# Kernel optimization log

Hardware: AMD Instinct MI355X
Metric: run time of the kernel (lower is better)

The kernel has to match this reference:

```python
import jax, jax.numpy as jnp
import numpy as np
import math

DIM = 1024
HEADS = 16
SEQ_LEN = 2048
NUM_PV = 32
HEAD_DIM = DIM // HEADS
EPS = 1e-5


def setup_inputs() -> dict:
    key = jax.random.key(0)
    k1, k2 = jax.random.split(key)
    B = 4
    L = SEQ_LEN + NUM_PV
    x = jax.random.normal(k1, (B, L, DIM), dtype=jnp.float32)
    paramvecs = jax.random.normal(k2, (1, NUM_PV, DIM), dtype=jnp.float32)
    return {"x": x, "paramvecs": paramvecs}


def _layernorm_noaffine(x):
    mu = jnp.mean(x, axis=-1, keepdims=True)
    var = jnp.mean(jnp.square(x - mu), axis=-1, keepdims=True)
    return (x - mu) * jax.lax.rsqrt(var + EPS)


def reference(x, paramvecs):
    B, L, D = x.shape  # L = SEQ_LEN + NUM_PV
    # add learned param vectors onto the trailing num_paramvec positions
    x = x.at[:, SEQ_LEN:, :].add(paramvecs)
    residual = x
    xn = _layernorm_noaffine(x)
    # shared Q = K = V = xn, split into heads: [B, H, L, Dh]
    h = xn.reshape(B, L, HEADS, HEAD_DIM).transpose(0, 2, 1, 3)
    scores = jnp.einsum('bhqd,bhkd->bhqk', h, h) / math.sqrt(HEAD_DIM)
    weights = jax.nn.softmax(scores, axis=-1)
    context = jnp.einsum('bhqk,bhkd->bhqd', weights, h)
    context = context.transpose(0, 2, 1, 3).reshape(B, L, D)
    return context + residual
```

## Files before the change

kernel.cpp:

```cpp
#include <hip/hip_runtime.h>
#include <hip/hip_fp16.h>

#define DIMF 1024
#define NHEADS 16
#define SEQ 2048
#define NPV 32
#define HD 64
#define LTOT 2080
#define LP 2112
#define NB 4
#define BHN 64
#define NQT 33
#define QB 128
#define NQB 17
#define NKV 65

typedef _Float16 f16x8 __attribute__((ext_vector_type(8)));
typedef float f32x16 __attribute__((ext_vector_type(16)));
typedef unsigned short u16x8 __attribute__((ext_vector_type(8)));
typedef int v2i __attribute__((ext_vector_type(2)));

#if __has_builtin(__builtin_amdgcn_exp2f)
#define EXP2(x) __builtin_amdgcn_exp2f(x)
#else
#define EXP2(x) exp2f(x)
#endif

#define CEXP 0.1803368801111f
#define KSH  11.5415603271f

__global__ __launch_bounds__(256) void prep_kernel(const float* __restrict__ x,
                                                   const float* __restrict__ pv,
                                                   float* __restrict__ out,
                                                   unsigned short* __restrict__ xnh) {
  int row = blockIdx.x;
  int b = row / LP, l = row - b * LP;
  int t = threadIdx.x;
  int h = t >> 4;
  int dd = (t & 15) << 2;
  unsigned short* dst = xnh + ((size_t)(b * NHEADS + h) * LP + l) * HD + dd;
  if (l >= LTOT) {
    *reinterpret_cast<ushort4*>(dst) = make_ushort4(0, 0, 0, 0);
    return;
  }
  const float* xr = x + ((size_t)b * LTOT + l) * DIMF + t * 4;
  float4 v = *reinterpret_cast<const float4*>(xr);
  if (l >= SEQ) {
    float4 p = *reinterpret_cast<const float4*>(pv + (size_t)(l - SEQ) * DIMF + t * 4);
    v.x += p.x; v.y += p.y; v.z += p.z; v.w += p.w;
  }
  *reinterpret_cast<float4*>(out + ((size_t)b * LTOT + l) * DIMF + t * 4) = v;

  float s1 = v.x + v.y + v.z + v.w;
  float s2 = v.x * v.x + v.y * v.y + v.z * v.z + v.w * v.w;
#pragma unroll
  for (int o = 1; o < 64; o <<= 1) { s1 += __shfl_xor(s1, o); s2 += __shfl_xor(s2, o); }
  __shared__ float red[8];
  int wv = t >> 6;
  if ((t & 63) == 0) { red[wv] = s1; red[4 + wv] = s2; }
  __syncthreads();
  s1 = red[0] + red[1] + red[2] + red[3];
  s2 = red[4] + red[5] + red[6] + red[7];
  float mu = s1 * (1.0f / DIMF);
  float var = s2 * (1.0f / DIMF) - mu * mu;
  float rs = rsqrtf(var + 1e-5f);
  ushort4 o4;
  o4.x = __half_as_ushort(__float2half((v.x - mu) * rs));
  o4.y = __half_as_ushort(__float2half((v.y - mu) * rs));
  o4.z = __half_as_ushort(__float2half((v.z - mu) * rs));
  o4.w = __half_as_ushort(__float2half((v.w - mu) * rs));
  *reinterpret_cast<ushort4*>(dst) = o4;
}

__global__ __launch_bounds__(256) void transpose_kernel(const unsigned short* __restrict__ xnh,
                                                        unsigned short* __restrict__ xnt) {
  __shared__ unsigned short tile[64][72];
  int blk = blockIdx.x;
  int bh = blk / NQT, lt = blk - bh * NQT;
  int t = threadIdx.x;
  int rr = t >> 3;
  int c8 = (t & 7) << 3;
#pragma unroll
  for (int p = 0; p < 2; p++) {
    int ll = rr + p * 32;
    float4 v = *reinterpret_cast<const float4*>(xnh + ((size_t)bh * LP + lt * 64 + ll) * HD + c8);
    int cs = c8 ^ (((ll >> 3) & 7) << 3);
    *reinterpret_cast<float4*>(&tile[ll][cs]) = v;
  }
  __syncthreads();
  int l8 = (t & 7) << 3;
#pragma unroll
  for (int p = 0; p < 2; p++) {
    int d = rr + p * 32;
    u16x8 o;
#pragma unroll
    for (int j = 0; j < 8; j++) {
      o[j] = tile[l8 + j][d ^ ((t & 7) << 3)];
    }
    *reinterpret_cast<u16x8*>(xnt + ((size_t)bh * HD + d) * LP + lt * 64 + l8) = o;
  }
}

static __device__ __forceinline__ f32x16 mfma32(f16x8 a, f16x8 b, f32x16 c) {
  return __builtin_amdgcn_mfma_f32_32x32x16_f16(a, b, c, 0, 0, 0);
}

static __device__ __forceinline__ unsigned cvtpk(float a, float b) {
  auto h = __builtin_amdgcn_cvt_pkrtz(a, b);
  return __builtin_bit_cast(unsigned, h);
}

static __device__ __forceinline__ void pack2(const f32x16& P, f16x8& f0, f16x8& f1) {
  unsigned a0 = cvtpk(P[0], P[1]),  b0 = cvtpk(P[4], P[5]);
  unsigned a1 = cvtpk(P[2], P[3]),  b1 = cvtpk(P[6], P[7]);
  v2i s0 = __builtin_amdgcn_permlane32_swap(a0, b0, false, false);
  v2i s1 = __builtin_amdgcn_permlane32_swap(a1, b1, false, false);
  unsigned a2 = cvtpk(P[8], P[9]),   b2 = cvtpk(P[12], P[13]);
  unsigned a3 = cvtpk(P[10], P[11]), b3 = cvtpk(P[14], P[15]);
  v2i s2 = __builtin_amdgcn_permlane32_swap(a2, b2, false, false);
  v2i s3 = __builtin_amdgcn_permlane32_swap(a3, b3, false, false);
  union { unsigned u[4]; f16x8 v; } u0, u1;
  u0.u[0] = (unsigned)s0.x; u0.u[1] = (unsigned)s1.x; u0.u[2] = (unsigned)s0.y; u0.u[3] = (unsigned)s1.y;
  u1.u[0] = (unsigned)s2.x; u1.u[1] = (unsigned)s3.x; u1.u[2] = (unsigned)s2.y; u1.u[3] = (unsigned)s3.y;
  f0 = u0.v; f1 = u1.v;
}

#define GLDS(src, dst) \
  __builtin_amdgcn_global_load_lds( \
      (const __attribute__((address_space(1))) unsigned int*)(src), \
      (__attribute__((address_space(3))) unsigned int*)(dst), 16, 0, 0)

__device__ __forceinline__ void kv_step16(const unsigned short* kbuf, const unsigned short* vbuf,
                                          const f16x8 (&qf)[4], f32x16& accA, f32x16& accB,
                                          float& rowsum, int l31, int hi, int sw) {
  const unsigned short* k0 = kbuf + (size_t)l31 * 64;
  f32x16 st;
#pragma unroll
  for (int r = 0; r < 16; r++) st[r] = -KSH;
  __builtin_amdgcn_s_setprio(1);
#pragma unroll
  for (int ds = 0; ds < 4; ds++) {
    int cl = ds * 2 + hi;
    f16x8 ka = *reinterpret_cast<const f16x8*>(k0 + ((cl ^ sw) << 3));
    st = mfma32(ka, qf[ds], st);
  }
  __builtin_amdgcn_s_setprio(0);
#pragma unroll
  for (int r = 0; r < 16; r++) {
    st[r] = EXP2(st[r]);
    rowsum += st[r];
  }
  f16x8 pa[2];
  pack2(st, pa[0], pa[1]);
  const unsigned short* v0 = vbuf + (size_t)l31 * 64;
  __builtin_amdgcn_s_setprio(1);
#pragma unroll
  for (int ks = 0; ks < 2; ks++) {
    int clA = ks * 2 + hi;
    f16x8 bvA = *reinterpret_cast<const f16x8*>(v0 + ((clA ^ sw) << 3));
    accA = mfma32(pa[ks], bvA, accA);
    int clB = 4 + ks * 2 + hi;
    f16x8 bvB = *reinterpret_cast<const f16x8*>(v0 + ((clB ^ sw) << 3));
    accB = mfma32(pa[ks], bvB, accB);
  }
  __builtin_amdgcn_s_setprio(0);
}

__global__ __launch_bounds__(256, 4) void attn_kernel(const unsigned short* __restrict__ xnh,
                                                      const unsigned short* __restrict__ xnt,
                                                      float* __restrict__ out) {
  __shared__ unsigned short kt0[32 * 64], kt1[32 * 64];
  __shared__ unsigned short vt0[32 * 64], vt1[32 * 64];
  __shared__ float wred[4][32];
  int bid = blockIdx.x;
  const int nwg = BHN * NQB;
  const int cpx = nwg >> 3;
  int wg = (bid & 7) * cpx + (bid >> 3);
  int bh = wg / NQB, qt = wg - bh * NQB;
  int b = bh >> 4, h = bh & 15;
  int tid = threadIdx.x;
  int wid = tid >> 6;
  int lane = tid & 63;
  int l31 = lane & 31, hi = lane >> 5;
  int sw = l31 & 7;
  int q0w = qt * QB + wid * 32;
  const unsigned short* Kb = xnh + (size_t)bh * (LP * HD);
  const unsigned short* Vb = xnt + (size_t)bh * (HD * LP);

  f16x8 qf[4];
  const _Float16 ce = (_Float16)CEXP;
  const f16x8 cev = {ce, ce, ce, ce, ce, ce, ce, ce};
#pragma unroll
  for (int ds = 0; ds < 4; ds++) {
    qf[ds] = *reinterpret_cast<const f16x8*>(Kb + (size_t)(q0w + l31) * HD + ds * 16 + hi * 8);
    qf[ds] = qf[ds] * cev;
  }

  f32x16 accA = {};
  f32x16 accB = {};
  float rowsum = 0.f;

  int r = tid >> 3, cp = tid & 7;
  int cl = cp ^ (r & 7);
  const unsigned short* pK = Kb + (size_t)r * HD + cl * 8;
  const unsigned short* pV = Vb + (size_t)(r + 32 * (cl >> 2)) * LP + (cl & 3) * 8;
  unsigned short* dK0 = kt0 + (size_t)wid * 512;
  unsigned short* dK1 = kt1 + (size_t)wid * 512;
  unsigned short* dV0 = vt0 + (size_t)wid * 512;
  unsigned short* dV1 = vt1 + (size_t)wid * 512;

#define STAGE0() do { GLDS(pK, dK0); GLDS(pV, dV0); pK += 32 * HD; pV += 32; } while (0)
#define STAGE1() do { GLDS(pK, dK1); GLDS(pV, dV1); pK += 32 * HD; pV += 32; } while (0)

  STAGE0();
  __syncthreads();

  for (int it = 0; it < 32; ++it) {
    STAGE1();
    kv_step16(kt0, vt0, qf, accA, accB, rowsum, l31, hi, sw);
    __syncthreads();
    STAGE0();
    kv_step16(kt1, vt1, qf, accA, accB, rowsum, l31, hi, sw);
    __syncthreads();
  }
  kv_step16(kt0, vt0, qf, accA, accB, rowsum, l31, hi, sw);

  float full = rowsum + __shfl_xor(rowsum, 32);
  float inv = 1.0f / full;
  if (lane < 32) wred[wid][l31] = inv;
  float* obase = out + (size_t)b * LTOT * DIMF + h * HD + l31;
  if (q0w < LTOT) {
#pragma unroll
    for (int q2 = 0; q2 < 4; q2++) {
      float4 iv = *reinterpret_cast<const float4*>(&wred[wid][q2 * 8 + hi * 4]);
#pragma unroll
      for (int j = 0; j < 4; j++) {
        int qg = q0w + q2 * 8 + hi * 4 + j;
        float* p = obase + (size_t)qg * DIMF;
        float ivj = (j == 0) ? iv.x : (j == 1) ? iv.y : (j == 2) ? iv.z : iv.w;
        p[0]  += accA[q2 * 4 + j] * ivj;
        p[32] += accB[q2 * 4 + j] * ivj;
      }
    }
  }
#undef STAGE0
#undef STAGE1
}

extern "C" void kernel_launch(void* const* d_in, const int* in_sizes, int n_in,
                              void* d_out, int out_size, void* d_ws, size_t ws_size,
                              hipStream_t stream) {
  const float* x  = (const float*)d_in[0];
  const float* pv = (const float*)d_in[1];
  float* out = (float*)d_out;
  unsigned short* xnh = (unsigned short*)d_ws;
  unsigned short* xnt = xnh + (size_t)BHN * LP * HD;
  prep_kernel<<<NB * LP, 256, 0, stream>>>(x, pv, out, xnh);
  transpose_kernel<<<BHN * NQT, 256, 0, stream>>>(xnh, xnt);
  attn_kernel<<<BHN * NQB, 256, 0, stream>>>(xnh, xnt, out);
}
```

Baseline: 121.4 us.

## Process two KV tiles per barrier with interleaved QK chains

```diff
diff --git a/kernel.cpp b/kernel.cpp
--- a/kernel.cpp
+++ b/kernel.cpp
@@ -130,21 +130,9 @@
       (const __attribute__((address_space(1))) unsigned int*)(src), \
       (__attribute__((address_space(3))) unsigned int*)(dst), 16, 0, 0)
 
-__device__ __forceinline__ void kv_step16(const unsigned short* kbuf, const unsigned short* vbuf,
-                                          const f16x8 (&qf)[4], f32x16& accA, f32x16& accB,
-                                          float& rowsum, int l31, int hi, int sw) {
-  const unsigned short* k0 = kbuf + (size_t)l31 * 64;
-  f32x16 st;
-#pragma unroll
-  for (int r = 0; r < 16; r++) st[r] = -KSH;
-  __builtin_amdgcn_s_setprio(1);
-#pragma unroll
-  for (int ds = 0; ds < 4; ds++) {
-    int cl = ds * 2 + hi;
-    f16x8 ka = *reinterpret_cast<const f16x8*>(k0 + ((cl ^ sw) << 3));
-    st = mfma32(ka, qf[ds], st);
-  }
-  __builtin_amdgcn_s_setprio(0);
+__device__ __forceinline__ void softmax_pv(f32x16& st, const unsigned short* v0,
+                                           f32x16& accA, f32x16& accB, float& rowsum,
+                                           int hi, int sw) {
 #pragma unroll
   for (int r = 0; r < 16; r++) {
     st[r] = EXP2(st[r]);
@@ -152,7 +140,6 @@
   }
   f16x8 pa[2];
   pack2(st, pa[0], pa[1]);
-  const unsigned short* v0 = vbuf + (size_t)l31 * 64;
   __builtin_amdgcn_s_setprio(1);
 #pragma unroll
   for (int ks = 0; ks < 2; ks++) {
@@ -166,11 +153,37 @@
   __builtin_amdgcn_s_setprio(0);
 }
 
+__device__ __forceinline__ f32x16 qk_chain(const unsigned short* k0, const f16x8 (&qf)[4],
+                                           const f32x16& kshC, int hi, int sw) {
+  f32x16 st;
+#pragma unroll
+  for (int ds = 0; ds < 4; ds++) {
+    int cl = ds * 2 + hi;
+    f16x8 ka = *reinterpret_cast<const f16x8*>(k0 + ((cl ^ sw) << 3));
+    st = mfma32(ka, qf[ds], ds == 0 ? kshC : st);
+  }
+  return st;
+}
+
+__device__ __forceinline__ void kv_pair(const unsigned short* kbuf, const unsigned short* vbuf,
+                                        const f16x8 (&qf)[4], const f32x16& kshC,
+                                        f32x16& accA, f32x16& accB,
+                                        float& rowsum, int l31, int hi, int sw) {
+  const unsigned short* k0 = kbuf + (size_t)l31 * 64;
+  const unsigned short* v0 = vbuf + (size_t)l31 * 64;
+  __builtin_amdgcn_s_setprio(1);
+  f32x16 st0 = qk_chain(k0, qf, kshC, hi, sw);
+  f32x16 st1 = qk_chain(k0 + 2048, qf, kshC, hi, sw);
+  __builtin_amdgcn_s_setprio(0);
+  softmax_pv(st0, v0, accA, accB, rowsum, hi, sw);
+  softmax_pv(st1, v0 + 2048, accA, accB, rowsum, hi, sw);
+}
+
 __global__ __launch_bounds__(256, 4) void attn_kernel(const unsigned short* __restrict__ xnh,
                                                       const unsigned short* __restrict__ xnt,
                                                       float* __restrict__ out) {
-  __shared__ unsigned short kt0[32 * 64], kt1[32 * 64];
-  __shared__ unsigned short vt0[32 * 64], vt1[32 * 64];
+  __shared__ unsigned short kA[2 * 2048], kB[2 * 2048];
+  __shared__ unsigned short vA[2 * 2048], vB[2 * 2048];
   __shared__ float wred[4][32];
   int bid = blockIdx.x;
   const int nwg = BHN * NQB;
@@ -195,6 +208,9 @@
     qf[ds] = *reinterpret_cast<const f16x8*>(Kb + (size_t)(q0w + l31) * HD + ds * 16 + hi * 8);
     qf[ds] = qf[ds] * cev;
   }
+  f32x16 kshC;
+#pragma unroll
+  for (int r = 0; r < 16; r++) kshC[r] = -KSH;
 
   f32x16 accA = {};
   f32x16 accB = {};
@@ -204,26 +220,31 @@
   int cl = cp ^ (r & 7);
   const unsigned short* pK = Kb + (size_t)r * HD + cl * 8;
   const unsigned short* pV = Vb + (size_t)(r + 32 * (cl >> 2)) * LP + (cl & 3) * 8;
-  unsigned short* dK0 = kt0 + (size_t)wid * 512;
-  unsigned short* dK1 = kt1 + (size_t)wid * 512;
-  unsigned short* dV0 = vt0 + (size_t)wid * 512;
-  unsigned short* dV1 = vt1 + (size_t)wid * 512;
-
-#define STAGE0() do { GLDS(pK, dK0); GLDS(pV, dV0); pK += 32 * HD; pV += 32; } while (0)
-#define STAGE1() do { GLDS(pK, dK1); GLDS(pV, dV1); pK += 32 * HD; pV += 32; } while (0)
-
-  STAGE0();
+  int wo = wid * 512;
+
+#define STAGEP(kb, vb) do { \
+    GLDS(pK, (kb) + wo); GLDS(pK + 2048, (kb) + 2048 + wo); \
+    GLDS(pV, (vb) + wo); GLDS(pV + 32, (vb) + 2048 + wo); \
+    pK += 4096; pV += 64; } while (0)
+
+  STAGEP(kA, vA);
   __syncthreads();
 
-  for (int it = 0; it < 32; ++it) {
-    STAGE1();
-    kv_step16(kt0, vt0, qf, accA, accB, rowsum, l31, hi, sw);
+  for (int it = 0; it < 16; ++it) {
+    STAGEP(kB, vB);
+    kv_pair(kA, vA, qf, kshC, accA, accB, rowsum, l31, hi, sw);
     __syncthreads();
-    STAGE0();
-    kv_step16(kt1, vt1, qf, accA, accB, rowsum, l31, hi, sw);
+    STAGEP(kA, vA);
+    kv_pair(kB, vB, qf, kshC, accA, accB, rowsum, l31, hi, sw);
     __syncthreads();
   }
-  kv_step16(kt0, vt0, qf, accA, accB, rowsum, l31, hi, sw);
+  {
+    const unsigned short* k0 = kA + (size_t)l31 * 64;
+    __builtin_amdgcn_s_setprio(1);
+    f32x16 st = qk_chain(k0, qf, kshC, hi, sw);
+    __builtin_amdgcn_s_setprio(0);
+    softmax_pv(st, vA + (size_t)l31 * 64, accA, accB, rowsum, hi, sw);
+  }
 
   float full = rowsum + __shfl_xor(rowsum, 32);
   float inv = 1.0f / full;
@@ -243,8 +264,7 @@
       }
     }
   }
-#undef STAGE0
-#undef STAGE1
+#undef STAGEP
 }
 
 extern "C" void kernel_launch(void* const* d_in, const int* in_sizes, int n_in,
```

Result: slower. 161.4 us (+33.0%).
